# Kernel tuning notes

Hardware: AMD Instinct MI355X
Metric: run time of the kernel (lower is better)

## Reference

```python
import jax, jax.numpy as jnp
import numpy as np

B, T, K, H = 8, 1024, 128, 8
TOP_K = 64
KS = 5  # conv kernel size for Q/K
DN = ('NCH', 'OIH', 'NCH')


def setup_inputs() -> dict:
    key = jax.random.key(0)
    ks = jax.random.split(key, 9)
    s = 0.05
    return {
        'x': jax.random.normal(ks[0], (B, T, K), jnp.float32),
        'Wq': jax.random.normal(ks[1], (K * H, K, KS), jnp.float32) * s,
        'bq': jax.random.normal(ks[2], (K * H,), jnp.float32) * s,
        'Wk': jax.random.normal(ks[3], (K * H, K, KS), jnp.float32) * s,
        'bk': jax.random.normal(ks[4], (K * H,), jnp.float32) * s,
        'Wv': jax.random.normal(ks[5], (K * H, K, 1), jnp.float32) * s,
        'bv': jax.random.normal(ks[6], (K * H,), jnp.float32) * s,
        'Wu': jax.random.normal(ks[7], (K, K * H), jnp.float32) * s,
        'bu': jax.random.normal(ks[8], (K,), jnp.float32) * s,
    }


def _prep(z, b, k, h, t, scale):
    # z: (b, k*h, t) conv output; torch view(b,k,h,t) then transposes -> (b,h,t,k)
    z = z.reshape(b, k, h, t)
    z = jnp.transpose(z, (0, 2, 3, 1)) * scale  # (b, h, t, k)
    # torch: transpose(1,2).contiguous().view(b*h, t, k) -- replicate exactly
    z = jnp.transpose(z, (0, 2, 1, 3)).reshape(b * h, t, k)
    return z


def reference(x, Wq, bq, Wk, bk, Wv, bv, Wu, bu):
    b, t, k = x.shape
    h = H
    xc = jnp.transpose(x, (0, 2, 1))  # (b, k, t)
    # causal left-pad KS-1 for Q/K convs; V is pointwise (kernel 1)
    q = jax.lax.conv_general_dilated(xc, Wq, (1,), [(KS - 1, 0)], dimension_numbers=DN) + bq[None, :, None]
    kk = jax.lax.conv_general_dilated(xc, Wk, (1,), [(KS - 1, 0)], dimension_numbers=DN) + bk[None, :, None]
    v = jax.lax.conv_general_dilated(xc, Wv, (1,), [(0, 0)], dimension_numbers=DN) + bv[None, :, None]
    scale = k ** -0.25
    q = _prep(q, b, k, h, t, scale)
    kk = _prep(kk, b, k, h, t, scale)
    v = _prep(v, b, k, h, t, 1.0)
    w = jnp.einsum('btk,bsk->bts', q, kk)  # (b*h, t, t)
    # top-k sparsification: keep entries >= k-th largest per row, else row min
    largest, _ = jax.lax.top_k(w, TOP_K)
    thresh = jnp.min(largest, axis=-1, keepdims=True)
    row_min = jnp.min(w, axis=-1, keepdims=True)
    w = jnp.where(w >= thresh, w, row_min)
    # causal mask (strict upper triangle -> -inf)
    causal = jnp.triu(jnp.ones((t, t), bool), 1)
    w = jnp.where(causal[None], -jnp.inf, w)
    w = jax.nn.softmax(w, axis=-1)
    out = jnp.einsum('bts,bsk->btk', w, v)  # (b*h, t, k)
    out = out.reshape(b, h, t, k)
    out = jnp.transpose(out, (0, 2, 1, 3)).reshape(b, t, k * h)
    return out @ Wu.T + bu
```

## Files before the change

### kernel.cpp

```cpp
#include <hip/hip_runtime.h>
#include <hip/hip_fp16.h>
#include <cstdint>

using f16 = _Float16;
typedef __attribute__((ext_vector_type(8))) _Float16 f16x8;
typedef __attribute__((ext_vector_type(4))) _Float16 f16x4;
typedef __attribute__((ext_vector_type(4))) float f32x4;

#define MFMA16(a, b, c) __builtin_amdgcn_mfma_f32_16x16x32_f16((a), (b), (c), 0, 0, 0)

__device__ __forceinline__ f16x8 ldfrag(const f16* p) { return *(const f16x8*)p; }

__device__ __forceinline__ void dma16(const f16* g, f16* l) {
  __builtin_amdgcn_global_load_lds(
      (const __attribute__((address_space(1))) void*)g,
      (__attribute__((address_space(3))) void*)l, 16, 0, 0);
}
__device__ __forceinline__ void wait_vm0() {
  asm volatile("s_waitcnt vmcnt(0)" ::: "memory");
}
__device__ __forceinline__ void wait_lgkm0() {
  asm volatile("s_waitcnt lgkmcnt(0)" ::: "memory");
}
__device__ __forceinline__ void wait_vm4() {
  asm volatile("s_waitcnt vmcnt(4)" ::: "memory");
}
__device__ __forceinline__ void wait_vm2() {
  asm volatile("s_waitcnt vmcnt(2)" ::: "memory");
}

static const int64_t NX = 1048576;
static const int64_t NW = 655360;
static const int64_t NV = 131072;

__global__ __launch_bounds__(256) void k0_prep(
    const float* __restrict__ x, const float* __restrict__ Wq,
    const float* __restrict__ Wk, const float* __restrict__ Wv,
    const float* __restrict__ Wu,
    f16* __restrict__ xh, f16* __restrict__ xl,
    f16* __restrict__ Wqh, f16* __restrict__ Wql,
    f16* __restrict__ Wkh, f16* __restrict__ Wkl,
    f16* __restrict__ Wvb, f16* __restrict__ Wub) {
  int64_t i = (int64_t)blockIdx.x * 256 + threadIdx.x;
  if (i < NX) {
    const float v = x[i];
    const f16 h = (f16)v;
    xh[i] = h; xl[i] = (f16)(v - (float)h);
  } else if (i < NX + NW) {
    int64_t d = i - NX;
    int j = (int)(d >> 17);
    int rem = (int)(d & 131071);
    int o = rem >> 7, c = rem & 127;
    const float v = Wq[(int64_t)(o * 128 + c) * 5 + j];
    const f16 h = (f16)v;
    Wqh[d] = h; Wql[d] = (f16)(v - (float)h);
  } else if (i < NX + 2 * NW) {
    int64_t d = i - NX - NW;
    int j = (int)(d >> 17);
    int rem = (int)(d & 131071);
    int o = rem >> 7, c = rem & 127;
    const float v = Wk[(int64_t)(o * 128 + c) * 5 + j];
    const f16 h = (f16)v;
    Wkh[d] = h; Wkl[d] = (f16)(v - (float)h);
  } else if (i < NX + 2 * NW + NV) {
    int64_t d = i - NX - 2 * NW;
    Wvb[d] = (f16)Wv[d];
  } else {
    int64_t d = i - NX - 2 * NW - NV;
    Wub[d] = (f16)Wu[d];
  }
}

#define STAGE_QK(DST, PASS, VALEXPR)                                    \
  {                                                                     \
    __syncthreads();                                                    \
    _Pragma("unroll")                                                   \
    for (int nt = 0; nt < 8; ++nt) {                                    \
      const int o = o0 + nt * 16 + lo;                                  \
      const int kcl = (o >> 3) & 63, hh = o & 7;                        \
      _Pragma("unroll")                                                 \
      for (int rtl = 0; rtl < 2; ++rtl) {                               \
        const int rt = (PASS) * 2 + rtl;                                \
        _Pragma("unroll")                                               \
        for (int r = 0; r < 4; ++r) {                                   \
          const int t2l = (rtl * 16 + quad * 4 + r) * 8 + hh;           \
          lds[t2l * 72 + kcl] = (VALEXPR);                              \
        }                                                               \
      }                                                                 \
    }                                                                   \
    __syncthreads();                                                    \
    _Pragma("unroll")                                                   \
    for (int p = 0; p < 8; ++p) {                                       \
      const int idx = p * 256 + tid;                                    \
      const int a = idx >> 3, c8 = (idx & 7) * 8;                       \
      *(f16x8*)(DST + ((int64_t)m * 1024 + t2b + (PASS) * 256 + a) * 128 + \
                half * 64 + c8) = *(const f16x8*)&lds[a * 72 + c8];     \
    }                                                                   \
  }

__global__ __launch_bounds__(256) void k1_conv(
    const f16* __restrict__ xh, const f16* __restrict__ xl,
    const f16* __restrict__ Wqh, const f16* __restrict__ Wql,
    const f16* __restrict__ Wkh, const f16* __restrict__ Wkl,
    const f16* __restrict__ Wvb,
    const float* __restrict__ bq, const float* __restrict__ bk,
    const float* __restrict__ bv,
    f16* __restrict__ q3h, f16* __restrict__ q3l,
    f16* __restrict__ k3h, f16* __restrict__ k3l,
    f16* __restrict__ v3T) {
  __shared__ f16 shm[36384];
  f16* const wbuf = shm;
  f16* const xbuf = shm + 18432;
  f16* const lds  = shm;
  const int tid = threadIdx.x;
  const int w = tid >> 6, lane = tid & 63;
  const int quad = lane >> 4, lo = lane & 15;
  const int r0 = blockIdx.x * 64;
  const int bb = r0 >> 10;
  const int m  = r0 >> 7;
  const int t2b = (r0 & 127) * 8;
  const int tloc = r0 & 1023;
  const int half = blockIdx.y;
  const int isK = blockIdx.z;
  const int o0 = half * 512 + w * 128;

  const f16* Wh = isK ? Wkh : Wqh;
  const f16* Wl = isK ? Wkl : Wql;
  const float* bias = isK ? bk : bq;

#pragma unroll
  for (int p = 0; p < 9; ++p) {
    const int u = p * 256 + tid;
    if (u < 2176) {
      const int row = u >> 5, tz = (u >> 4) & 1, c8 = (u & 15) * 8;
      int lt = tloc - 4 + row;
      if (lt < 0) lt = 0;
      const f16* src = (tz ? xl : xh) + ((int64_t)(bb * 1024 + lt)) * 128 + c8;
      *(f16x8*)&xbuf[row * 264 + tz * 128 + c8] = *(const f16x8*)src;
    }
  }
  __syncthreads();

  const int64_t wlane = (int64_t)(lane & 15) * 128 + (lane >> 4) * 8;

  if (!isK) {
    f32x4 av[4][8];
#pragma unroll
    for (int rt = 0; rt < 4; ++rt)
#pragma unroll
      for (int i = 0; i < 8; ++i)
#pragma unroll
        for (int r = 0; r < 4; ++r) av[rt][i][r] = 0.f;

#pragma unroll
    for (int g = 0; g < 4; ++g) {
#pragma unroll
      for (int s = 0; s < 2; ++s) {
        const int64_t vsrc = (int64_t)(o0 + (g * 2 + s) * 16) * 128 + wlane;
#pragma unroll
        for (int kk = 0; kk < 4; ++kk)
          dma16(Wvb + vsrc + kk * 32, wbuf + w * 4096 + s * 2048 + kk * 512);
      }
      wait_vm0();
#pragma unroll
      for (int kk = 0; kk < 4; ++kk) {
        f16x8 a[4];
#pragma unroll
        for (int rt = 0; rt < 4; ++rt)
          a[rt] = *(const f16x8*)&xbuf[(rt * 16 + lo + 4) * 264 + kk * 32 +
                                       quad * 8];
#pragma unroll
        for (int s = 0; s < 2; ++s) {
          const f16x8 bv8 = *(const f16x8*)&wbuf[w * 4096 + s * 2048 + kk * 512 +
                                                 quad * 128 + lo * 8];
#pragma unroll
          for (int rt = 0; rt < 4; ++rt)
            av[rt][g * 2 + s] = MFMA16(a[rt], bv8, av[rt][g * 2 + s]);
        }
      }
      wait_lgkm0();
    }
    __syncthreads();
#pragma unroll
    for (int pass = 0; pass < 2; ++pass) {
#pragma unroll
      for (int nt = 0; nt < 8; ++nt) {
        const int o = o0 + nt * 16 + lo;
        const float vbv = bv[o];
        const int kcl = (o >> 3) & 63, hh = o & 7;
#pragma unroll
        for (int rtl = 0; rtl < 2; ++rtl)
#pragma unroll
          for (int r = 0; r < 4; ++r) {
            const int t2l = (rtl * 16 + quad * 4 + r) * 8 + hh;
            lds[kcl * 264 + t2l] = (f16)(av[pass * 2 + rtl][nt][r] + vbv);
          }
      }
      __syncthreads();
#pragma unroll
      for (int p = 0; p < 8; ++p) {
        const int idx = p * 256 + tid;
        const int kcl = idx >> 5, t8 = (idx & 31) * 8;
        *(f16x8*)(v3T + ((int64_t)m * 128 + half * 64 + kcl) * 1024 + t2b +
                  pass * 256 + t8) = *(const f16x8*)&lds[kcl * 264 + t8];
      }
      __syncthreads();
    }
  }

  f32x4 aq[4][8];
#pragma unroll
  for (int rt = 0; rt < 4; ++rt)
#pragma unroll
    for (int i = 0; i < 8; ++i)
#pragma unroll
      for (int r = 0; r < 4; ++r) { aq[rt][i][r] = 0.f; }

  const int64_t wbase = wlane + (int64_t)o0 * 128;
#define ISSUE_HALF(J, KK, NTG, H)                                       \
  {                                                                     \
    _Pragma("unroll")                                                   \
    for (int ntl2 = 0; ntl2 < 2; ++ntl2) {                              \
      const int ntl_ = (H) * 2 + ntl2;                                  \
      const int64_t o_ = wbase + (int64_t)(J) * 131072 + (KK) * 32 +    \
                         (int64_t)(((NTG) * 4 + ntl_) * 16) * 128;      \
      dma16(Wh + o_, wbuf + w * 4096 + ntl_ * 1024);                    \
      dma16(Wl + o_, wbuf + w * 4096 + ntl_ * 1024 + 512);              \
    }                                                                   \
  }

  ISSUE_HALF(0, 0, 0, 0)
  ISSUE_HALF(0, 0, 0, 1)

  const bool z0 = (tloc == 0);
  for (int j = 0; j < 5; ++j) {
    f16x8 ah[4], al[4];
#pragma unroll
    for (int c = 0; c < 8; ++c) {
      const int kk = c >> 1, ntg = c & 1;
      if (ntg == 0) {
#pragma unroll
        for (int rt = 0; rt < 4; ++rt) {
          ah[rt] = *(const f16x8*)&xbuf[(rt * 16 + lo + j) * 264 + kk * 32 +
                                        quad * 8];
          al[rt] = *(const f16x8*)&xbuf[(rt * 16 + lo + j) * 264 + 128 +
                                        kk * 32 + quad * 8];
        }
        if (z0 && (lo + j < 4)) {
#pragma unroll
          for (int e = 0; e < 8; ++e) { ah[0][e] = (f16)0; al[0][e] = (f16)0; }
        }
      }
      const int nj = (c == 7) ? j + 1 : j;
      const int nkk = (c == 7) ? 0 : ((c + 1) >> 1);
      const int nntg = (c == 7) ? 0 : ((c + 1) & 1);
      const bool more = (c < 7) || (j < 4);

      wait_vm4();
#pragma unroll
      for (int ntl = 0; ntl < 2; ++ntl) {
        const int nt = ntg * 4 + ntl;
        const f16x8 bh = *(const f16x8*)&wbuf[w * 4096 + ntl * 1024 +
                                              quad * 128 + lo * 8];
        const f16x8 bl = *(const f16x8*)&wbuf[w * 4096 + ntl * 1024 + 512 +
                                              quad * 128 + lo * 8];
#pragma unroll
        for (int rt = 0; rt < 4; ++rt) {
          aq[rt][nt] = MFMA16(ah[rt], bh, aq[rt][nt]);
          aq[rt][nt] = MFMA16(ah[rt], bl, aq[rt][nt]);
          aq[rt][nt] = MFMA16(al[rt], bh, aq[rt][nt]);
        }
      }
      wait_lgkm0();
      if (more) ISSUE_HALF(nj, nkk, nntg, 0)

      if (c == 7) {
        if (j == 4) wait_vm0(); else wait_vm4();
      } else {
        wait_vm4();
      }
#pragma unroll
      for (int ntl = 2; ntl < 4; ++ntl) {
        const int nt = ntg * 4 + ntl;
        const f16x8 bh = *(const f16x8*)&wbuf[w * 4096 + ntl * 1024 +
                                              quad * 128 + lo * 8];
        const f16x8 bl = *(const f16x8*)&wbuf[w * 4096 + ntl * 1024 + 512 +
                                              quad * 128 + lo * 8];
#pragma unroll
        for (int rt = 0; rt < 4; ++rt) {
          aq[rt][nt] = MFMA16(ah[rt], bh, aq[rt][nt]);
          aq[rt][nt] = MFMA16(ah[rt], bl, aq[rt][nt]);
          aq[rt][nt] = MFMA16(al[rt], bh, aq[rt][nt]);
        }
      }
      wait_lgkm0();
      if (more) ISSUE_HALF(nj, nkk, nntg, 1)
    }
  }
#undef ISSUE_HALF

  const float SC = 0.29730177875068026f;
#pragma unroll
  for (int nt = 0; nt < 8; ++nt) {
    const int o = o0 + nt * 16 + lo;
    const float vb = bias[o];
#pragma unroll
    for (int rt = 0; rt < 4; ++rt)
#pragma unroll
      for (int r = 0; r < 4; ++r) aq[rt][nt][r] = (aq[rt][nt][r] + vb) * SC;
  }

  if (!isK) {
    STAGE_QK(q3h, 0, (f16)aq[rt][nt][r])
    STAGE_QK(q3h, 1, (f16)aq[rt][nt][r])
    STAGE_QK(q3l, 0, (f16)(aq[rt][nt][r] - (float)(f16)aq[rt][nt][r]))
    STAGE_QK(q3l, 1, (f16)(aq[rt][nt][r] - (float)(f16)aq[rt][nt][r]))
  } else {
    STAGE_QK(k3h, 0, (f16)aq[rt][nt][r])
    STAGE_QK(k3h, 1, (f16)aq[rt][nt][r])
    STAGE_QK(k3l, 0, (f16)(aq[rt][nt][r] - (float)(f16)aq[rt][nt][r]))
    STAGE_QK(k3l, 1, (f16)(aq[rt][nt][r] - (float)(f16)aq[rt][nt][r]))
  }
}

__global__ __launch_bounds__(512, 4) void k234_attn(
    const f16* __restrict__ q3h, const f16* __restrict__ q3l,
    const f16* __restrict__ k3h, const f16* __restrict__ k3l,
    const f16* __restrict__ v3T, f16* __restrict__ A) {
  __shared__ float Sb[16 * 516];
  __shared__ f16 kbuf[16384];
  __shared__ f16 qlds[4096];
  const int tid = threadIdx.x;
  const int w = tid >> 6, lane = tid & 63;
  const int quad = lane >> 4, lo = lane & 15;
  const int qd = lane & 3, cit = lane >> 2;
  const int qsw = qd ^ ((cit >> 1) & 3);
  const int fro = (lo * 4 + (quad ^ ((lo >> 1) & 3))) * 8;
  const int hid = blockIdx.y * 32 + blockIdx.x;
  const int m = (hid & 7) * 8 + ((hid >> 3) >> 5);
  const int r0 = ((hid >> 3) & 31) * 32;

  unsigned key[2][2][16];
  unsigned kmn[2][2];
#pragma unroll
  for (int g = 0; g < 2; ++g)
#pragma unroll
    for (int rr = 0; rr < 2; ++rr) kmn[g][rr] = 0xFFFFFFFFu;

#pragma unroll
  for (int half = 0; half < 2; ++half) {
    f32x4 acc[2][4];
#pragma unroll
    for (int g = 0; g < 2; ++g)
#pragma unroll
      for (int i = 0; i < 4; ++i)
#pragma unroll
        for (int r = 0; r < 4; ++r) acc[g][i][r] = 0.f;

    for (int kp = 0; kp < 2; ++kp) {
      __syncthreads();
      {
        const int h_ = w & 1, grp_ = (w >> 1) & 1, kkhs = (w >> 2) & 1;
        const f16* qsrc = (h_ ? q3l : q3h) +
            ((int64_t)m * 1024 + r0 + grp_ * 16 + lo) * 128 +
            (kp * 2 + kkhs) * 32 + quad * 8;
        dma16(qsrc, qlds + w * 512);
        wait_vm0();
      }
      __syncthreads();

#pragma unroll
      for (int cc = 0; cc < 4; ++cc) {
        const int c0 = half * 512 + cc * 128;
        const int64_t rowg = (int64_t)(m * 1024 + c0 + w * 16 + cit) * 128;
#pragma unroll
        for (int t = 0; t < 2; ++t) {
          const f16* srcb = t ? k3l : k3h;
#pragma unroll
          for (int kkh = 0; kkh < 2; ++kkh)
            dma16(srcb + rowg + (kp * 2 + kkh) * 32 + qsw * 8,
                  kbuf + (w * 4 + t * 2 + kkh) * 512);
        }
        wait_vm0();
#pragma unroll
        for (int kkh = 0; kkh < 2; ++kkh) {
          const f16x8 qh0 = ldfrag(qlds + (kkh * 4 + 0) * 512 + lane * 8);
          const f16x8 ql0 = ldfrag(qlds + (kkh * 4 + 1) * 512 + lane * 8);
          const f16x8 qh1 = ldfrag(qlds + (kkh * 4 + 2) * 512 + lane * 8);
          const f16x8 ql1 = ldfrag(qlds + (kkh * 4 + 3) * 512 + lane * 8);
          const f16x8 bh = *(const f16x8*)(kbuf + (w * 4 + kkh) * 512 + fro);
          const f16x8 bl =
              *(const f16x8*)(kbuf + (w * 4 + 2 + kkh) * 512 + fro);
          acc[0][cc] = MFMA16(qh0, bh, acc[0][cc]);
          acc[0][cc] = MFMA16(qh0, bl, acc[0][cc]);
          acc[0][cc] = MFMA16(ql0, bh, acc[0][cc]);
          acc[1][cc] = MFMA16(qh1, bh, acc[1][cc]);
          acc[1][cc] = MFMA16(qh1, bl, acc[1][cc]);
          acc[1][cc] = MFMA16(ql1, bh, acc[1][cc]);
        }
        wait_lgkm0();
      }
    }

#pragma unroll
    for (int grp = 0; grp < 2; ++grp) {
#pragma unroll
      for (int cc = 0; cc < 4; ++cc)
#pragma unroll
        for (int r = 0; r < 4; ++r)
          Sb[(quad * 4 + r) * 516 + cc * 128 + w * 16 + lo] = acc[grp][cc][r];
      __syncthreads();
#pragma unroll
      for (int rr = 0; rr < 2; ++rr) {
        const float4* rp = (const float4*)(Sb + (w * 2 + rr) * 516);
#pragma unroll
        for (int i2 = 0; i2 < 2; ++i2) {
          const float4 f4 = rp[i2 * 64 + lane];
          const float fe[4] = {f4.x, f4.y, f4.z, f4.w};
#pragma unroll
          for (int e = 0; e < 4; ++e) {
            const unsigned u = __builtin_bit_cast(unsigned, fe[e]);
            const unsigned k = (u & 0x80000000u) ? ~u : (u | 0x80000000u);
            key[grp][rr][half * 8 + i2 * 4 + e] = k;
            kmn[grp][rr] = min(kmn[grp][rr], k);
          }
        }
      }
      __syncthreads();
    }
  }

  const int64_t vrow = (int64_t)(m * 128 + w * 16 + cit) * 1024;
#define VISSUE(KB, PAIR)                                                 \
  {                                                                      \
    dma16(v3T + vrow + (KB) * 64 + qsw * 8,                              \
          kbuf + (w * 4 + (PAIR) * 2) * 512);                            \
    dma16(v3T + vrow + (KB) * 64 + 32 + qsw * 8,                         \
          kbuf + (w * 4 + (PAIR) * 2 + 1) * 512);                        \
  }
  VISSUE(0, 0)
  if (r0 >= 64) VISSUE(1, 1)

#pragma unroll
  for (int off = 32; off; off >>= 1) {
#pragma unroll
    for (int g = 0; g < 2; ++g)
#pragma unroll
      for (int rr = 0; rr < 2; ++rr)
        kmn[g][rr] = min(kmn[g][rr],
                         (unsigned)__shfl_xor((int)kmn[g][rr], off));
  }
  unsigned th[2][2] = {{0u, 0u}, {0u, 0u}};
  {
    bool dn[2][2] = {{false, false}, {false, false}};
    for (int b = 31; b >= 0; --b) {
      bool all = true;
#pragma unroll
      for (int g = 0; g < 2; ++g)
#pragma unroll
        for (int rr = 0; rr < 2; ++rr) {
          if (!dn[g][rr]) {
            const unsigned c = th[g][rr] | (1u << b);
            int cnt = 0;
#pragma unroll
            for (int i = 0; i < 16; ++i)
              cnt += (int)__popcll(__ballot(key[g][rr][i] >= c));
            if (cnt >= 64) { th[g][rr] = c; if (cnt == 64) dn[g][rr] = true; }
          }
          all = all && dn[g][rr];
        }
      if (all) break;
    }
  }

  f16* P16 = (f16*)Sb;
#pragma unroll
  for (int grp = 0; grp < 2; ++grp) {
    const int nkb = ((r0 + grp * 16) >> 6) + 1;
    if (grp == 1) __syncthreads();
#pragma unroll
    for (int rr = 0; rr < 2; ++rr) {
      const unsigned kth = th[grp][rr];
      const unsigned kmv = kmn[grp][rr];
      const int row = w * 2 + rr, t2 = r0 + grp * 16 + row;
      const unsigned umn = (kmv & 0x80000000u) ? (kmv ^ 0x80000000u) : ~kmv;
      const float mn = __builtin_bit_cast(float, umn);
      const unsigned ukv = (kth & 0x80000000u) ? (kth ^ 0x80000000u) : ~kth;
      const float kv = __builtin_bit_cast(float, ukv);

      float ev[16];
      float sum = 0.f;
#pragma unroll
      for (int j = 0; j < 16; ++j) {
        const int s = (j >> 3) * 512 + ((j >> 2) & 1) * 256 + lane * 4 + (j & 3);
        const unsigned k = key[grp][rr][j];
        const unsigned uu = (k & 0x80000000u) ? (k ^ 0x80000000u) : ~k;
        const float f = __builtin_bit_cast(float, uu);
        const float ww = (k >= kth) ? f : mn;
        const float x = (s <= t2) ? __expf(ww - kv) : 0.f;
        ev[j] = x;
        sum += x;
      }
      for (int off = 32; off; off >>= 1) sum += __shfl_xor(sum, off);
      const float inv = 1.0f / sum;

      f16* prow = P16 + row * 1032;
#pragma unroll
      for (int hh = 0; hh < 2; ++hh)
#pragma unroll
        for (int i2 = 0; i2 < 2; ++i2) {
          f16x4 pk;
#pragma unroll
          for (int e = 0; e < 4; ++e)
            pk[e] = (f16)(ev[hh * 8 + i2 * 4 + e] * inv);
          *(f16x4*)(prow + hh * 512 + i2 * 256 + lane * 4) = pk;
        }
    }
    __syncthreads();

    f32x4 oa0, oa1;
#pragma unroll
    for (int r = 0; r < 4; ++r) { oa0[r] = 0.f; oa1[r] = 0.f; }
    for (int kb = 0; kb < nkb; ++kb) {
      if (kb + 1 < nkb) wait_vm2();
      else wait_vm0();
      const int pair = kb & 1;
      {
        const f16x8 vf0 =
            *(const f16x8*)(kbuf + (w * 4 + pair * 2) * 512 + fro);
        const f16x8 vf1 =
            *(const f16x8*)(kbuf + (w * 4 + pair * 2 + 1) * 512 + fro);
        const f16x8 af0 = *(const f16x8*)(P16 + lo * 1032 + kb * 64 + quad * 8);
        const f16x8 af1 =
            *(const f16x8*)(P16 + lo * 1032 + kb * 64 + 32 + quad * 8);
        oa0 = MFMA16(af0, vf0, oa0);
        oa1 = MFMA16(af1, vf1, oa1);
      }
      wait_lgkm0();
      if (kb + 2 < nkb) VISSUE(kb + 2, pair)
    }
    if (grp == 0) {
      VISSUE(0, 0)
      if (((r0 + 16) >> 6) + 1 > 1) VISSUE(1, 1)
    }
#pragma unroll
    for (int r = 0; r < 4; ++r)
      A[((int64_t)m * 1024 + r0 + grp * 16 + quad * 4 + r) * 128 + w * 16 +
        lo] = (f16)(oa0[r] + oa1[r]);
  }
#undef VISSUE
}

__global__ __launch_bounds__(256) void k5_proj(
    const f16* __restrict__ A, const f16* __restrict__ Wub,
    const float* __restrict__ bu, float* __restrict__ out) {
  const int w = threadIdx.x >> 6, lane = threadIdx.x & 63;
  const int quad = lane >> 4, lo = lane & 15;
  const int rt = w & 1, ch = w >> 1;
  const int r0 = blockIdx.x * 32 + rt * 16;
  const int r = r0 + lo;
  const int bI = r >> 10, t2 = r & 1023;

  f32x4 acc[4];
#pragma unroll
  for (int i = 0; i < 4; ++i)
#pragma unroll
    for (int rr = 0; rr < 4; ++rr) acc[i][rr] = 0.f;

#pragma unroll 2
  for (int kk = 0; kk < 32; ++kk) {
    const int o = kk * 32 + quad * 8;
    const int j = o >> 7, kc = o & 127;
    f16x8 a = ldfrag(A + (((int64_t)(bI * 8 + j) * 1024 + t2) * 128 + kc));
    f16x8 wb[4];
#pragma unroll
    for (int nt = 0; nt < 4; ++nt)
      wb[nt] = ldfrag(Wub + (int64_t)(ch * 64 + nt * 16 + lo) * 1024 + o);
#pragma unroll
    for (int nt = 0; nt < 4; ++nt) acc[nt] = MFMA16(a, wb[nt], acc[nt]);
  }
#pragma unroll
  for (int nt = 0; nt < 4; ++nt) {
    const int col = ch * 64 + nt * 16 + lo;
    const float bias = bu[col];
#pragma unroll
    for (int rr = 0; rr < 4; ++rr) {
      const int row = r0 + quad * 4 + rr;
      out[(int64_t)row * 128 + col] = acc[nt][rr] + bias;
    }
  }
}

extern "C" void kernel_launch(void* const* d_in, const int* in_sizes, int n_in,
                              void* d_out, int out_size, void* d_ws, size_t ws_size,
                              hipStream_t stream) {
  const float* x  = (const float*)d_in[0];
  const float* Wq = (const float*)d_in[1];
  const float* bq = (const float*)d_in[2];
  const float* Wk = (const float*)d_in[3];
  const float* bk = (const float*)d_in[4];
  const float* Wv = (const float*)d_in[5];
  const float* bv = (const float*)d_in[6];
  const float* Wu = (const float*)d_in[7];
  const float* bu = (const float*)d_in[8];
  float* out = (float*)d_out;

  char* ws = (char*)d_ws;
  f16* xh  = (f16*)ws;  ws += 2097152;
  f16* xl  = (f16*)ws;  ws += 2097152;
  f16* Wqh = (f16*)ws;  ws += 1310720;
  f16* Wql = (f16*)ws;  ws += 1310720;
  f16* Wkh = (f16*)ws;  ws += 1310720;
  f16* Wkl = (f16*)ws;  ws += 1310720;
  f16* Wvb = (f16*)ws;  ws += 262144;
  f16* Wub = (f16*)ws;  ws += 262144;
  f16* q3h = (f16*)ws;  ws += 16777216;
  f16* q3l = (f16*)ws;  ws += 16777216;
  f16* k3h = (f16*)ws;  ws += 16777216;
  f16* k3l = (f16*)ws;  ws += 16777216;
  f16* v3T = (f16*)ws;  ws += 16777216;
  f16* A   = (f16*)ws;  ws += 16777216;

  k0_prep<<<10240, 256, 0, stream>>>(x, Wq, Wk, Wv, Wu,
                                     xh, xl, Wqh, Wql, Wkh, Wkl, Wvb, Wub);

  k1_conv<<<dim3(128, 2, 2), 256, 0, stream>>>(xh, xl, Wqh, Wql, Wkh, Wkl, Wvb,
                                               bq, bk, bv, q3h, q3l, k3h, k3l,
                                               v3T);

  k234_attn<<<dim3(32, 64), 512, 0, stream>>>(q3h, q3l, k3h, k3l, v3T, A);

  k5_proj<<<256, 256, 0, stream>>>(A, Wub, bu, out);

  (void)in_sizes; (void)n_in; (void)out_size; (void)ws_size;
}
```

Before: 389.5 us.

## Shrink attention LDS footprint and double-buffer K tile loads

Merges the score buffer, probability buffer, K/V staging and Q staging into one shared-memory arena. The score and probability buffers are halved by staging scores in two column quarters and writing probabilities in two 512-column passes, so LDS use drops from about 66KB to about 54KB per block. The QK loop now loads Q per 32-wide k-slice and double-buffers K tiles with partial waits, overlapping DMA with MFMA. The cost is extra barriers and a second P write/PV pass for rows past 512, and the code is more complex.

Result: no change. 393.7 us (+1.1%).

```diff
diff --git a/kernel.cpp b/kernel.cpp
--- a/kernel.cpp
+++ b/kernel.cpp
@@ -327,9 +327,11 @@
     const f16* __restrict__ q3h, const f16* __restrict__ q3l,
     const f16* __restrict__ k3h, const f16* __restrict__ k3l,
     const f16* __restrict__ v3T, f16* __restrict__ A) {
-  __shared__ float Sb[16 * 516];
-  __shared__ f16 kbuf[16384];
-  __shared__ f16 qlds[4096];
+  __shared__ __align__(16) char smem[54016];
+  float* const SbQ = (float*)smem;
+  f16* const Pbuf = (f16*)smem;
+  f16* const kbuf = (f16*)(smem + 17152);
+  f16* const qlds = (f16*)(smem + 17152 + 32768);
   const int tid = threadIdx.x;
   const int w = tid >> 6, lane = tid & 63;
   const int quad = lane >> 4, lo = lane & 15;
@@ -358,75 +360,82 @@
         for (int r = 0; r < 4; ++r) acc[g][i][r] = 0.f;
 
     for (int kp = 0; kp < 2; ++kp) {
-      __syncthreads();
-      {
-        const int h_ = w & 1, grp_ = (w >> 1) & 1, kkhs = (w >> 2) & 1;
-        const f16* qsrc = (h_ ? q3l : q3h) +
-            ((int64_t)m * 1024 + r0 + grp_ * 16 + lo) * 128 +
-            (kp * 2 + kkhs) * 32 + quad * 8;
-        dma16(qsrc, qlds + w * 512);
+#pragma unroll
+      for (int kkh = 0; kkh < 2; ++kkh) {
+        __syncthreads();
+        if (w < 4) {
+          const int h_ = w & 1, grp_ = w >> 1;
+          const f16* qsrc = (h_ ? q3l : q3h) +
+              ((int64_t)m * 1024 + r0 + grp_ * 16 + lo) * 128 +
+              (kp * 2 + kkh) * 32 + quad * 8;
+          dma16(qsrc, qlds + w * 512);
+        }
         wait_vm0();
-      }
-      __syncthreads();
-
-#pragma unroll
-      for (int cc = 0; cc < 4; ++cc) {
-        const int c0 = half * 512 + cc * 128;
-        const int64_t rowg = (int64_t)(m * 1024 + c0 + w * 16 + cit) * 128;
-#pragma unroll
-        for (int t = 0; t < 2; ++t) {
-          const f16* srcb = t ? k3l : k3h;
-#pragma unroll
-          for (int kkh = 0; kkh < 2; ++kkh)
-            dma16(srcb + rowg + (kp * 2 + kkh) * 32 + qsw * 8,
-                  kbuf + (w * 4 + t * 2 + kkh) * 512);
-        }
-        wait_vm0();
-#pragma unroll
-        for (int kkh = 0; kkh < 2; ++kkh) {
-          const f16x8 qh0 = ldfrag(qlds + (kkh * 4 + 0) * 512 + lane * 8);
-          const f16x8 ql0 = ldfrag(qlds + (kkh * 4 + 1) * 512 + lane * 8);
-          const f16x8 qh1 = ldfrag(qlds + (kkh * 4 + 2) * 512 + lane * 8);
-          const f16x8 ql1 = ldfrag(qlds + (kkh * 4 + 3) * 512 + lane * 8);
-          const f16x8 bh = *(const f16x8*)(kbuf + (w * 4 + kkh) * 512 + fro);
+        __syncthreads();
+
+#define KISS(CC, PAIR)                                                   \
+  {                                                                      \
+    const int64_t rowg =                                                 \
+        (int64_t)(m * 1024 + half * 512 + (CC) * 128 + w * 16 + cit) *   \
+            128 + (kp * 2 + kkh) * 32 + qsw * 8;                         \
+    dma16(k3h + rowg, kbuf + (w * 4 + (PAIR) * 2) * 512);                \
+    dma16(k3l + rowg, kbuf + (w * 4 + (PAIR) * 2 + 1) * 512);            \
+  }
+        KISS(0, 0)
+        KISS(1, 1)
+#pragma unroll
+        for (int cc = 0; cc < 4; ++cc) {
+          if (cc < 3) wait_vm2();
+          else wait_vm0();
+          const int pair = cc & 1;
+          const f16x8 qh0 = ldfrag(qlds + 0 * 512 + lane * 8);
+          const f16x8 ql0 = ldfrag(qlds + 1 * 512 + lane * 8);
+          const f16x8 qh1 = ldfrag(qlds + 2 * 512 + lane * 8);
+          const f16x8 ql1 = ldfrag(qlds + 3 * 512 + lane * 8);
+          const f16x8 bh =
+              *(const f16x8*)(kbuf + (w * 4 + pair * 2) * 512 + fro);
           const f16x8 bl =
-              *(const f16x8*)(kbuf + (w * 4 + 2 + kkh) * 512 + fro);
+              *(const f16x8*)(kbuf + (w * 4 + pair * 2 + 1) * 512 + fro);
           acc[0][cc] = MFMA16(qh0, bh, acc[0][cc]);
           acc[0][cc] = MFMA16(qh0, bl, acc[0][cc]);
           acc[0][cc] = MFMA16(ql0, bh, acc[0][cc]);
           acc[1][cc] = MFMA16(qh1, bh, acc[1][cc]);
           acc[1][cc] = MFMA16(qh1, bl, acc[1][cc]);
           acc[1][cc] = MFMA16(ql1, bh, acc[1][cc]);
-        }
-        wait_lgkm0();
+          wait_lgkm0();
+          if (cc == 0) KISS(2, 0)
+          if (cc == 1) KISS(3, 1)
+        }
+#undef KISS
       }
     }
 
 #pragma unroll
     for (int grp = 0; grp < 2; ++grp) {
 #pragma unroll
-      for (int cc = 0; cc < 4; ++cc)
-#pragma unroll
-        for (int r = 0; r < 4; ++r)
-          Sb[(quad * 4 + r) * 516 + cc * 128 + w * 16 + lo] = acc[grp][cc][r];
-      __syncthreads();
-#pragma unroll
-      for (int rr = 0; rr < 2; ++rr) {
-        const float4* rp = (const float4*)(Sb + (w * 2 + rr) * 516);
-#pragma unroll
-        for (int i2 = 0; i2 < 2; ++i2) {
-          const float4 f4 = rp[i2 * 64 + lane];
+      for (int q = 0; q < 2; ++q) {
+#pragma unroll
+        for (int c2 = 0; c2 < 2; ++c2)
+#pragma unroll
+          for (int r = 0; r < 4; ++r)
+            SbQ[(quad * 4 + r) * 268 + c2 * 128 + w * 16 + lo] =
+                acc[grp][q * 2 + c2][r];
+        __syncthreads();
+#pragma unroll
+        for (int rr = 0; rr < 2; ++rr) {
+          const float4 f4 =
+              *(const float4*)(SbQ + (w * 2 + rr) * 268 + lane * 4);
           const float fe[4] = {f4.x, f4.y, f4.z, f4.w};
 #pragma unroll
           for (int e = 0; e < 4; ++e) {
             const unsigned u = __builtin_bit_cast(unsigned, fe[e]);
             const unsigned k = (u & 0x80000000u) ? ~u : (u | 0x80000000u);
-            key[grp][rr][half * 8 + i2 * 4 + e] = k;
+            key[grp][rr][half * 8 + q * 4 + e] = k;
             kmn[grp][rr] = min(kmn[grp][rr], k);
           }
         }
-      }
-      __syncthreads();
+        __syncthreads();
+      }
     }
   }
 
@@ -473,56 +482,58 @@
     }
   }
 
-  f16* P16 = (f16*)Sb;
 #pragma unroll
   for (int grp = 0; grp < 2; ++grp) {
     const int nkb = ((r0 + grp * 16) >> 6) + 1;
+    const int nkb0 = nkb < 8 ? nkb : 8;
     if (grp == 1) __syncthreads();
+
+    float ev[2][16];
+    float inv[2];
 #pragma unroll
     for (int rr = 0; rr < 2; ++rr) {
       const unsigned kth = th[grp][rr];
       const unsigned kmv = kmn[grp][rr];
-      const int row = w * 2 + rr, t2 = r0 + grp * 16 + row;
+      const int t2 = r0 + grp * 16 + w * 2 + rr;
       const unsigned umn = (kmv & 0x80000000u) ? (kmv ^ 0x80000000u) : ~kmv;
       const float mn = __builtin_bit_cast(float, umn);
       const unsigned ukv = (kth & 0x80000000u) ? (kth ^ 0x80000000u) : ~kth;
       const float kv = __builtin_bit_cast(float, ukv);
-
-      float ev[16];
       float sum = 0.f;
 #pragma unroll
       for (int j = 0; j < 16; ++j) {
-        const int s = (j >> 3) * 512 + ((j >> 2) & 1) * 256 + lane * 4 + (j & 3);
+        const int s = (j >> 2) * 256 + lane * 4 + (j & 3);
         const unsigned k = key[grp][rr][j];
         const unsigned uu = (k & 0x80000000u) ? (k ^ 0x80000000u) : ~k;
         const float f = __builtin_bit_cast(float, uu);
         const float ww = (k >= kth) ? f : mn;
         const float x = (s <= t2) ? __expf(ww - kv) : 0.f;
-        ev[j] = x;
+        ev[rr][j] = x;
         sum += x;
       }
       for (int off = 32; off; off >>= 1) sum += __shfl_xor(sum, off);
-      const float inv = 1.0f / sum;
-
-      f16* prow = P16 + row * 1032;
-#pragma unroll
-      for (int hh = 0; hh < 2; ++hh)
-#pragma unroll
-        for (int i2 = 0; i2 < 2; ++i2) {
-          f16x4 pk;
-#pragma unroll
-          for (int e = 0; e < 4; ++e)
-            pk[e] = (f16)(ev[hh * 8 + i2 * 4 + e] * inv);
-          *(f16x4*)(prow + hh * 512 + i2 * 256 + lane * 4) = pk;
-        }
+      inv[rr] = 1.0f / sum;
+    }
+
+#pragma unroll
+    for (int rr = 0; rr < 2; ++rr) {
+      f16* prow = Pbuf + (w * 2 + rr) * 520;
+#pragma unroll
+      for (int i2 = 0; i2 < 2; ++i2) {
+        f16x4 pk;
+#pragma unroll
+        for (int e = 0; e < 4; ++e)
+          pk[e] = (f16)(ev[rr][i2 * 4 + e] * inv[rr]);
+        *(f16x4*)(prow + i2 * 256 + lane * 4) = pk;
+      }
     }
     __syncthreads();
 
     f32x4 oa0, oa1;
 #pragma unroll
     for (int r = 0; r < 4; ++r) { oa0[r] = 0.f; oa1[r] = 0.f; }
-    for (int kb = 0; kb < nkb; ++kb) {
-      if (kb + 1 < nkb) wait_vm2();
+    for (int kb = 0; kb < nkb0; ++kb) {
+      if (kb + 1 < nkb0) wait_vm2();
       else wait_vm0();
       const int pair = kb & 1;
       {
@@ -530,15 +541,54 @@
             *(const f16x8*)(kbuf + (w * 4 + pair * 2) * 512 + fro);
         const f16x8 vf1 =
             *(const f16x8*)(kbuf + (w * 4 + pair * 2 + 1) * 512 + fro);
-        const f16x8 af0 = *(const f16x8*)(P16 + lo * 1032 + kb * 64 + quad * 8);
+        const f16x8 af0 = *(const f16x8*)(Pbuf + lo * 520 + kb * 64 + quad * 8);
         const f16x8 af1 =
-            *(const f16x8*)(P16 + lo * 1032 + kb * 64 + 32 + quad * 8);
+            *(const f16x8*)(Pbuf + lo * 520 + kb * 64 + 32 + quad * 8);
         oa0 = MFMA16(af0, vf0, oa0);
         oa1 = MFMA16(af1, vf1, oa1);
       }
       wait_lgkm0();
-      if (kb + 2 < nkb) VISSUE(kb + 2, pair)
-    }
+      if (kb + 2 < nkb0) VISSUE(kb + 2, pair)
+    }
+
+    if (nkb > 8) {
+      VISSUE(8, 0)
+      if (nkb > 9) VISSUE(9, 1)
+      __syncthreads();
+#pragma unroll
+      for (int rr = 0; rr < 2; ++rr) {
+        f16* prow = Pbuf + (w * 2 + rr) * 520;
+#pragma unroll
+        for (int i2 = 0; i2 < 2; ++i2) {
+          f16x4 pk;
+#pragma unroll
+          for (int e = 0; e < 4; ++e)
+            pk[e] = (f16)(ev[rr][8 + i2 * 4 + e] * inv[rr]);
+          *(f16x4*)(prow + i2 * 256 + lane * 4) = pk;
+        }
+      }
+      __syncthreads();
+      for (int kb = 8; kb < nkb; ++kb) {
+        if (kb + 1 < nkb) wait_vm2();
+        else wait_vm0();
+        const int pair = kb & 1;
+        {
+          const f16x8 vf0 =
+              *(const f16x8*)(kbuf + (w * 4 + pair * 2) * 512 + fro);
+          const f16x8 vf1 =
+              *(const f16x8*)(kbuf + (w * 4 + pair * 2 + 1) * 512 + fro);
+          const f16x8 af0 =
+              *(const f16x8*)(Pbuf + lo * 520 + (kb - 8) * 64 + quad * 8);
+          const f16x8 af1 =
+              *(const f16x8*)(Pbuf + lo * 520 + (kb - 8) * 64 + 32 + quad * 8);
+          oa0 = MFMA16(af0, vf0, oa0);
+          oa1 = MFMA16(af1, vf1, oa1);
+        }
+        wait_lgkm0();
+        if (kb + 2 < nkb) VISSUE(kb + 2, pair)
+      }
+    }
+
     if (grp == 0) {
       VISSUE(0, 0)
       if (((r0 + 16) >> 6) + 1 > 1) VISSUE(1, 1)
```
